# Performance work log

Measured on AMD Instinct MI355X. Metric: run time of the kernel, lower is better.

## Reference

```python
import jax, jax.numpy as jnp
import numpy as np

B, S, D, H = 2, 2048, 1024, 16
DH = D // H  # 64


def setup_inputs() -> dict:
    key = jax.random.key(0)
    ks = jax.random.split(key, 9)
    def rn(k, shape, scale=1.0):
        return jax.random.normal(k, shape, dtype=jnp.float32) * scale
    w_scale = 1.0 / np.sqrt(D)
    return {
        "queries": rn(ks[0], (B, S, D)),
        "keys": rn(ks[1], (B, S, D)),
        "values": rn(ks[2], (B, S, D)),
        "Wq": rn(ks[3], (D, D), w_scale),
        "bq": rn(ks[4], (D,), w_scale),
        "Wk": rn(ks[5], (D, D), w_scale),
        "bk": rn(ks[6], (D,), w_scale),
        "Wv": rn(ks[7], (D, D), w_scale),
        "bv": rn(ks[8], (D,), w_scale),
    }


def _split_heads(x):
    # torch: cat(split(x, DH, dim=-1), dim=0) -> index (h*B + b); equivalent to
    # [B,S,H,DH] -> [H,B,S,DH]
    bsz, slen, _ = x.shape
    return x.reshape(bsz, slen, H, DH).transpose(2, 0, 1, 3)


def reference(queries, keys, values, Wq, bq, Wk, bk, Wv, bv):
    # Linear projections (W stored so that y = x @ W + b)
    Q = queries @ Wq + bq
    K = keys @ Wk + bk
    V = values @ Wv + bv

    Qh = _split_heads(Q)  # [H,B,S,DH]
    Kh = _split_heads(K)
    Vh = _split_heads(V)

    scale = 1.0 / jnp.sqrt(jnp.asarray(DH, dtype=Qh.dtype))
    scores = jnp.einsum("hbqd,hbkd->hbqk", Qh, Kh) * scale  # [H,B,S,S]
    attn = jax.nn.softmax(scores, axis=-1)  # dropout_rate=0 -> identity
    out = jnp.einsum("hbqk,hbkd->hbqd", attn, Vh)  # [H,B,S,DH]

    # torch: cat(split(out, B, dim=0), dim=2) -> [B,S,H*DH] with head h in slice h
    out = out.transpose(1, 2, 0, 3).reshape(queries.shape[0], queries.shape[1], D)
    return out + queries  # residual; NOTE: W_O is defined but unused in the original forward
```

## Files before the change

### kernel.cpp

```cpp
#include <hip/hip_runtime.h>
#include <hip/hip_bf16.h>
#include <math.h>

#define BB 2
#define SS 2048
#define DD 1024
#define HH 16
#define DHH 64
#define MM (BB * SS)

typedef float f32x4 __attribute__((ext_vector_type(4)));
typedef float f32x16 __attribute__((ext_vector_type(16)));
typedef __bf16 bf16x8 __attribute__((ext_vector_type(8)));

#define N_QKV ((size_t)MM * DD)
#define N_W   ((size_t)DD * DD)

__device__ unsigned short g_X [3][N_QKV];
__device__ unsigned short g_Q [N_QKV];
__device__ unsigned short g_K [N_QKV];
__device__ unsigned short g_Vt[N_QKV];
__device__ unsigned short g_Wt[3][N_W];

__device__ __forceinline__ unsigned short f2bu(float f) {
    unsigned u = __float_as_uint(f);
    unsigned r = u + 0x7FFFu + ((u >> 16) & 1u);
    return (unsigned short)(r >> 16);
}

union FragU { uint4 u; bf16x8 v; unsigned short s[8]; };
static __device__ __forceinline__ bf16x8 ldfrag(const unsigned short* p) {
    FragU f; f.u = *(const uint4*)p; return f.v;
}

static __device__ __forceinline__ unsigned pkbf(float a, float b) {
    union { __bf16 h[2]; unsigned u; } w;
    w.h[0] = (__bf16)a; w.h[1] = (__bf16)b;
    return w.u;
}

__global__ __launch_bounds__(256) void cvt3(
        const float* __restrict__ x0, const float* __restrict__ x1,
        const float* __restrict__ x2, unsigned short* __restrict__ X)
{
    const float* src = blockIdx.y == 0 ? x0 : (blockIdx.y == 1 ? x1 : x2);
    unsigned short* dst = X + (size_t)blockIdx.y * N_QKV;
    const size_t i = ((size_t)blockIdx.x * 256 + threadIdx.x) * 4;
    const float4 v = *(const float4*)(src + i);
    ushort4 s;
    s.x = f2bu(v.x); s.y = f2bu(v.y); s.z = f2bu(v.z); s.w = f2bu(v.w);
    *(ushort4*)(dst + i) = s;
}

__global__ __launch_bounds__(256) void transpose_w3(
        const float* __restrict__ W0, const float* __restrict__ W1,
        const float* __restrict__ W2, unsigned short* __restrict__ Wt3)
{
    const float* W = blockIdx.z == 0 ? W0 : (blockIdx.z == 1 ? W1 : W2);
    unsigned short* Wt = Wt3 + (size_t)blockIdx.z * N_W;
    __shared__ float Ts[64][65];
    const int t = threadIdx.x;
    const int k0 = blockIdx.y * 64, n0 = blockIdx.x * 64;
#pragma unroll
    for (int i = 0; i < 16; ++i) {
        const int f = t + 256 * i, r = f >> 6, c = f & 63;
        Ts[r][c] = W[(size_t)(k0 + r) * DD + n0 + c];
    }
    __syncthreads();
#pragma unroll
    for (int i = 0; i < 16; ++i) {
        const int f = t + 256 * i, r = f >> 6, c = f & 63;
        Wt[(size_t)(n0 + r) * DD + k0 + c] = f2bu(Ts[c][r]);
    }
}

__global__ __launch_bounds__(256) void proj3(
        const unsigned short* __restrict__ X, const unsigned short* __restrict__ Wt3,
        const float* __restrict__ bq, const float* __restrict__ bk,
        const float* __restrict__ bv,
        unsigned short* __restrict__ Qp, unsigned short* __restrict__ Kp,
        unsigned short* __restrict__ Vtp)
{
    const int z = blockIdx.z;
    const unsigned short* xb = X   + (size_t)z * N_QKV;
    const unsigned short* Wt = Wt3 + (size_t)z * N_W;
    const float* bias = z == 0 ? bq : (z == 1 ? bk : bv);
    const float scale = z == 0 ? 0.18033688011112042f : 1.0f;

    __shared__ unsigned short As[128][72];
    __shared__ unsigned short Bs[128][72];
    const int t = threadIdx.x, lane = t & 63, w = t >> 6;
    const int q = lane >> 4, li = lane & 15;
    const int wm = (w >> 1) * 64, wn = (w & 1) * 64;
    const int m0 = blockIdx.y * 128, n0 = blockIdx.x * 128;
    const int rs = t >> 3, cs = (t & 7) * 8;

    f32x4 acc[4][4];
#pragma unroll
    for (int mt = 0; mt < 4; ++mt)
#pragma unroll
        for (int nt = 0; nt < 4; ++nt) acc[mt][nt] = (f32x4)0.f;

    uint4 pa0, pa1, pa2, pa3, pb0, pb1, pb2, pb3;
#define PROJ_LD(kk) \
    pa0 = *(const uint4*)(xb + (size_t)(m0 + rs      ) * DD + (kk) + cs); \
    pa1 = *(const uint4*)(xb + (size_t)(m0 + rs + 32 ) * DD + (kk) + cs); \
    pa2 = *(const uint4*)(xb + (size_t)(m0 + rs + 64 ) * DD + (kk) + cs); \
    pa3 = *(const uint4*)(xb + (size_t)(m0 + rs + 96 ) * DD + (kk) + cs); \
    pb0 = *(const uint4*)(Wt + (size_t)(n0 + rs      ) * DD + (kk) + cs); \
    pb1 = *(const uint4*)(Wt + (size_t)(n0 + rs + 32 ) * DD + (kk) + cs); \
    pb2 = *(const uint4*)(Wt + (size_t)(n0 + rs + 64 ) * DD + (kk) + cs); \
    pb3 = *(const uint4*)(Wt + (size_t)(n0 + rs + 96 ) * DD + (kk) + cs);

    PROJ_LD(0)

    for (int kk = 0; kk < DD; kk += 64) {
        *(uint4*)&As[rs     ][cs] = pa0;
        *(uint4*)&As[rs + 32][cs] = pa1;
        *(uint4*)&As[rs + 64][cs] = pa2;
        *(uint4*)&As[rs + 96][cs] = pa3;
        *(uint4*)&Bs[rs     ][cs] = pb0;
        *(uint4*)&Bs[rs + 32][cs] = pb1;
        *(uint4*)&Bs[rs + 64][cs] = pb2;
        *(uint4*)&Bs[rs + 96][cs] = pb3;
        __syncthreads();
        if (kk + 64 < DD) { PROJ_LD(kk + 64) }
#pragma unroll
        for (int ks = 0; ks < 64; ks += 32) {
            bf16x8 a[4], b[4];
#pragma unroll
            for (int mt = 0; mt < 4; ++mt) a[mt] = ldfrag(&As[wm + mt * 16 + li][ks + q * 8]);
#pragma unroll
            for (int nt = 0; nt < 4; ++nt) b[nt] = ldfrag(&Bs[wn + nt * 16 + li][ks + q * 8]);
#pragma unroll
            for (int mt = 0; mt < 4; ++mt)
#pragma unroll
                for (int nt = 0; nt < 4; ++nt)
                    acc[mt][nt] = __builtin_amdgcn_mfma_f32_16x16x32_bf16(
                        a[mt], b[nt], acc[mt][nt], 0, 0, 0);
        }
        __syncthreads();
    }
#undef PROJ_LD

    float bvv[4];
#pragma unroll
    for (int nt = 0; nt < 4; ++nt) bvv[nt] = bias[n0 + wn + nt * 16 + li];

    if (z < 2) {
        unsigned short* out = z == 0 ? Qp : Kp;
#pragma unroll
        for (int mt = 0; mt < 4; ++mt)
#pragma unroll
            for (int nt = 0; nt < 4; ++nt)
#pragma unroll
                for (int reg = 0; reg < 4; ++reg) {
                    const int m = m0 + wm + mt * 16 + q * 4 + reg;
                    out[(size_t)m * DD + n0 + wn + nt * 16 + li] =
                        f2bu((acc[mt][nt][reg] + bvv[nt]) * scale);
                }
    } else {
        const int b = m0 >> 11;
        const int h = (n0 + wn) >> 6;
#pragma unroll
        for (int mt = 0; mt < 4; ++mt)
#pragma unroll
            for (int nt = 0; nt < 4; ++nt) {
                const int s = (m0 & (SS - 1)) + wm + mt * 16 + q * 4;
                const int dh = nt * 16 + li;
                ushort4 sv;
                sv.x = f2bu(acc[mt][nt][0] + bvv[nt]);
                sv.y = f2bu(acc[mt][nt][1] + bvv[nt]);
                sv.z = f2bu(acc[mt][nt][2] + bvv[nt]);
                sv.w = f2bu(acc[mt][nt][3] + bvv[nt]);
                *(ushort4*)(Vtp + ((size_t)((b * HH + h) * DHH + dh)) * SS + s) = sv;
            }
    }
}

__global__ __launch_bounds__(256) void attn5(
        const unsigned short* __restrict__ Qg, const unsigned short* __restrict__ Kg,
        const unsigned short* __restrict__ Vtg,
        const float* __restrict__ queries, float* __restrict__ outp)
{
    __shared__ unsigned short Kb[2][64][64];
    __shared__ unsigned short Vb[2][64][64];
    __shared__ float invL[4][32];

    const int t = threadIdx.x, lane = t & 63, w = t >> 6;
    const int col = lane & 31;
    const int hi  = lane >> 5;
    const int qt = blockIdx.x, h = blockIdx.y, b = blockIdx.z;

    const int sr = t >> 3;
    const int sc = t & 7;

    const unsigned short* Kbase = Kg  + (size_t)(b * SS) * DD + h * DHH;
    const unsigned short* Vbase = Vtg + ((size_t)((b * HH + h) * DHH)) * SS;

    bf16x8 qa[4];
    {
        const unsigned short* qp =
            Qg + (size_t)(b * SS + qt * 128 + w * 32 + col) * DD + h * DHH + hi * 8;
#pragma unroll
        for (int i = 0; i < 4; ++i) qa[i] = ldfrag(qp + i * 16);
    }

    f32x16 o0 = (f32x16)0.f, o1 = (f32x16)0.f;
    float lsum = 0.f;

    uint4 k0, k1, v0, v1;
#define LD_TILE(s0) \
    k0 = *(const uint4*)(Kbase + (size_t)((s0) + sr     ) * DD + sc * 8); \
    k1 = *(const uint4*)(Kbase + (size_t)((s0) + sr + 32) * DD + sc * 8); \
    v0 = *(const uint4*)(Vbase + (size_t)(sr     ) * SS + (s0) + sc * 8); \
    v1 = *(const uint4*)(Vbase + (size_t)(sr + 32) * SS + (s0) + sc * 8);

#define ST_TILE(buf) \
    *(uint4*)&Kb[buf][sr     ][(sc ^ (sr & 7)) * 8] = k0; \
    *(uint4*)&Kb[buf][sr + 32][(sc ^ (sr & 7)) * 8] = k1; \
    *(uint4*)&Vb[buf][sr     ][(sc ^ (sr & 7)) * 8] = v0; \
    *(uint4*)&Vb[buf][sr + 32][(sc ^ (sr & 7)) * 8] = v1;

    LD_TILE(0)
    ST_TILE(0)
    __syncthreads();

    const int NT = SS / 64;
    for (int kt = 0; kt < NT; ++kt) {
        const int cur = kt & 1;
        if (kt + 1 < NT) { LD_TILE((kt + 1) * 64) }

#pragma unroll
        for (int ksub = 0; ksub < 2; ++ksub) {
            f32x16 st = (f32x16)0.f;
            const int krow = ksub * 32 + col;
#pragma unroll
            for (int i = 0; i < 4; ++i) {
                bf16x8 ka = ldfrag(&Kb[cur][krow][((i * 2 + hi) ^ (krow & 7)) * 8]);
                st = __builtin_amdgcn_mfma_f32_32x32x16_bf16(ka, qa[i], st, 0, 0, 0);
            }

            float pe[16];
#pragma unroll
            for (int r = 0; r < 16; ++r) { pe[r] = exp2f(st[r]); lsum += pe[r]; }

            unsigned wl[2][2], wh[2][2];
#pragma unroll
            for (int s = 0; s < 2; ++s) {
                wl[s][0] = pkbf(pe[8 * s + 0], pe[8 * s + 1]);
                wl[s][1] = pkbf(pe[8 * s + 2], pe[8 * s + 3]);
                wh[s][0] = pkbf(pe[8 * s + 4], pe[8 * s + 5]);
                wh[s][1] = pkbf(pe[8 * s + 6], pe[8 * s + 7]);
            }

            if (ksub == 0 && kt + 1 < NT) { ST_TILE(cur ^ 1) }

#pragma unroll
            for (int s = 0; s < 2; ++s) {
                const unsigned self0 = hi ? wh[s][0] : wl[s][0];
                const unsigned self1 = hi ? wh[s][1] : wl[s][1];
                const unsigned send0 = hi ? wl[s][0] : wh[s][0];
                const unsigned send1 = hi ? wl[s][1] : wh[s][1];
                const unsigned r0 = (unsigned)__shfl_xor((int)send0, 32);
                const unsigned r1 = (unsigned)__shfl_xor((int)send1, 32);
                FragU pf;
                pf.u.x = hi ? r0 : self0;
                pf.u.y = hi ? r1 : self1;
                pf.u.z = hi ? self0 : r0;
                pf.u.w = hi ? self1 : r1;

                const int vslot = ksub * 4 + s * 2 + hi;
                bf16x8 vb0 = ldfrag(&Vb[cur][col     ][(vslot ^ (col & 7)) * 8]);
                bf16x8 vb1 = ldfrag(&Vb[cur][col + 32][(vslot ^ (col & 7)) * 8]);
                o0 = __builtin_amdgcn_mfma_f32_32x32x16_bf16(pf.v, vb0, o0, 0, 0, 0);
                o1 = __builtin_amdgcn_mfma_f32_32x32x16_bf16(pf.v, vb1, o1, 0, 0, 0);
            }
        }
        __syncthreads();
    }
#undef LD_TILE
#undef ST_TILE

    const float lt = lsum + __shfl_xor(lsum, 32);
    if (lane < 32) invL[w][lane] = 1.f / lt;
    __syncthreads();

    const size_t gbase = (size_t)(b * SS + qt * 128 + w * 32) * DD + h * DHH + col;
#pragma unroll
    for (int reg = 0; reg < 16; ++reg) {
        const int rl = (reg & 3) + 8 * (reg >> 2) + 4 * hi;
        const float inv = invL[w][rl];
        const size_t g = gbase + (size_t)rl * DD;
        outp[g]      = o0[reg] * inv + queries[g];
        outp[g + 32] = o1[reg] * inv + queries[g + 32];
    }
}

extern "C" void kernel_launch(void* const* d_in, const int* in_sizes, int n_in,
                              void* d_out, int out_size, void* d_ws, size_t ws_size,
                              hipStream_t stream) {
    const float* queries = (const float*)d_in[0];
    const float* keys    = (const float*)d_in[1];
    const float* values  = (const float*)d_in[2];
    const float* Wq      = (const float*)d_in[3];
    const float* bq      = (const float*)d_in[4];
    const float* Wk      = (const float*)d_in[5];
    const float* bk      = (const float*)d_in[6];
    const float* Wv      = (const float*)d_in[7];
    const float* bv      = (const float*)d_in[8];
    float* outp = (float*)d_out;

    const size_t need = (6 * N_QKV + 3 * N_W) * sizeof(unsigned short);
    unsigned short *Xp, *Qp, *Kp, *Vtp, *Wtp;
    if (ws_size >= need) {
        Xp  = (unsigned short*)d_ws;
        Qp  = Xp + 3 * N_QKV;
        Kp  = Qp + N_QKV;
        Vtp = Kp + N_QKV;
        Wtp = Vtp + N_QKV;
    } else {
        hipGetSymbolAddress((void**)&Xp,  HIP_SYMBOL(g_X));
        hipGetSymbolAddress((void**)&Qp,  HIP_SYMBOL(g_Q));
        hipGetSymbolAddress((void**)&Kp,  HIP_SYMBOL(g_K));
        hipGetSymbolAddress((void**)&Vtp, HIP_SYMBOL(g_Vt));
        hipGetSymbolAddress((void**)&Wtp, HIP_SYMBOL(g_Wt));
    }

    const dim3 bp(256);
    cvt3<<<dim3(MM * DD / 1024, 3), bp, 0, stream>>>(queries, keys, values, Xp);
    transpose_w3<<<dim3(16, 16, 3), bp, 0, stream>>>(Wq, Wk, Wv, Wtp);
    proj3<<<dim3(8, 32, 3), bp, 0, stream>>>(Xp, Wtp, bq, bk, bv, Qp, Kp, Vtp);
    attn5<<<dim3(SS / 128, HH, BB), bp, 0, stream>>>(Qp, Kp, Vtp, queries, outp);
}
```

Baseline: 220.6 us.

## Restructure attention inner loop with paired QK MFMAs and permlane32 swaps

```diff
diff --git a/kernel.cpp b/kernel.cpp
--- a/kernel.cpp
+++ b/kernel.cpp
@@ -12,6 +12,7 @@
 typedef float f32x4 __attribute__((ext_vector_type(4)));
 typedef float f32x16 __attribute__((ext_vector_type(16)));
 typedef __bf16 bf16x8 __attribute__((ext_vector_type(8)));
+typedef unsigned int u32x2 __attribute__((ext_vector_type(2)));
 
 #define N_QKV ((size_t)MM * DD)
 #define N_W   ((size_t)DD * DD)
@@ -37,6 +38,28 @@
     union { __bf16 h[2]; unsigned u; } w;
     w.h[0] = (__bf16)a; w.h[1] = (__bf16)b;
     return w.u;
+}
+
+static __device__ __forceinline__ float fexp2(float x) {
+#if __has_builtin(__builtin_amdgcn_exp2f)
+    return __builtin_amdgcn_exp2f(x);
+#else
+    return __expf(x * 0.6931471805599453f);
+#endif
+}
+
+static __device__ __forceinline__ void plswap(unsigned &a, unsigned &b) {
+#if __has_builtin(__builtin_amdgcn_permlane32_swap)
+    u32x2 r = __builtin_amdgcn_permlane32_swap((int)a, (int)b, false, false);
+    a = r[0]; b = r[1];
+#else
+    const bool hi = (threadIdx.x & 63) >= 32;
+    unsigned x = hi ? a : b;
+    unsigned y = (unsigned)__shfl_xor((int)x, 32);
+    unsigned na = hi ? y : a;
+    unsigned nb = hi ? b : y;
+    a = na; b = nb;
+#endif
 }
 
 __global__ __launch_bounds__(256) void cvt3(
@@ -178,7 +201,7 @@
     }
 }
 
-__global__ __launch_bounds__(256) void attn5(
+__global__ __launch_bounds__(256) void attn6(
         const unsigned short* __restrict__ Qg, const unsigned short* __restrict__ Kg,
         const unsigned short* __restrict__ Vtg,
         const float* __restrict__ queries, float* __restrict__ outp)
@@ -208,6 +231,7 @@
 
     f32x16 o0 = (f32x16)0.f, o1 = (f32x16)0.f;
     float lsum = 0.f;
+    const int xr = col & 7;
 
     uint4 k0, k1, v0, v1;
 #define LD_TILE(s0) \
@@ -227,55 +251,61 @@
     __syncthreads();
 
     const int NT = SS / 64;
+#pragma unroll 2
     for (int kt = 0; kt < NT; ++kt) {
         const int cur = kt & 1;
         if (kt + 1 < NT) { LD_TILE((kt + 1) * 64) }
 
-#pragma unroll
-        for (int ksub = 0; ksub < 2; ++ksub) {
-            f32x16 st = (f32x16)0.f;
-            const int krow = ksub * 32 + col;
-#pragma unroll
-            for (int i = 0; i < 4; ++i) {
-                bf16x8 ka = ldfrag(&Kb[cur][krow][((i * 2 + hi) ^ (krow & 7)) * 8]);
-                st = __builtin_amdgcn_mfma_f32_32x32x16_bf16(ka, qa[i], st, 0, 0, 0);
+        f32x16 st0 = (f32x16)0.f, st1 = (f32x16)0.f;
+#pragma unroll
+        for (int i = 0; i < 4; ++i) {
+            const int slot = ((i * 2 + hi) ^ xr) * 8;
+            bf16x8 ka0 = ldfrag(&Kb[cur][col     ][slot]);
+            bf16x8 ka1 = ldfrag(&Kb[cur][col + 32][slot]);
+            st0 = __builtin_amdgcn_mfma_f32_32x32x16_bf16(ka0, qa[i], st0, 0, 0, 0);
+            st1 = __builtin_amdgcn_mfma_f32_32x32x16_bf16(ka1, qa[i], st1, 0, 0, 0);
+        }
+
+        unsigned pkw[4][4];
+        {
+            float pe0[16], pe1[16];
+#pragma unroll
+            for (int r = 0; r < 16; ++r) { pe0[r] = fexp2(st0[r]); }
+#pragma unroll
+            for (int r = 0; r < 16; ++r) { pe1[r] = fexp2(st1[r]); }
+            float ls = 0.f;
+#pragma unroll
+            for (int r = 0; r < 16; ++r) ls += pe0[r] + pe1[r];
+            lsum += ls;
+#pragma unroll
+            for (int s = 0; s < 2; ++s) {
+                pkw[s][0]     = pkbf(pe0[8 * s + 0], pe0[8 * s + 1]);
+                pkw[s][1]     = pkbf(pe0[8 * s + 2], pe0[8 * s + 3]);
+                pkw[s][2]     = pkbf(pe0[8 * s + 4], pe0[8 * s + 5]);
+                pkw[s][3]     = pkbf(pe0[8 * s + 6], pe0[8 * s + 7]);
+                pkw[2 + s][0] = pkbf(pe1[8 * s + 0], pe1[8 * s + 1]);
+                pkw[2 + s][1] = pkbf(pe1[8 * s + 2], pe1[8 * s + 3]);
+                pkw[2 + s][2] = pkbf(pe1[8 * s + 4], pe1[8 * s + 5]);
+                pkw[2 + s][3] = pkbf(pe1[8 * s + 6], pe1[8 * s + 7]);
             }
-
-            float pe[16];
-#pragma unroll
-            for (int r = 0; r < 16; ++r) { pe[r] = exp2f(st[r]); lsum += pe[r]; }
-
-            unsigned wl[2][2], wh[2][2];
-#pragma unroll
-            for (int s = 0; s < 2; ++s) {
-                wl[s][0] = pkbf(pe[8 * s + 0], pe[8 * s + 1]);
-                wl[s][1] = pkbf(pe[8 * s + 2], pe[8 * s + 3]);
-                wh[s][0] = pkbf(pe[8 * s + 4], pe[8 * s + 5]);
-                wh[s][1] = pkbf(pe[8 * s + 6], pe[8 * s + 7]);
-            }
-
-            if (ksub == 0 && kt + 1 < NT) { ST_TILE(cur ^ 1) }
-
-#pragma unroll
-            for (int s = 0; s < 2; ++s) {
-                const unsigned self0 = hi ? wh[s][0] : wl[s][0];
-                const unsigned self1 = hi ? wh[s][1] : wl[s][1];
-                const unsigned send0 = hi ? wl[s][0] : wh[s][0];
-                const unsigned send1 = hi ? wl[s][1] : wh[s][1];
-                const unsigned r0 = (unsigned)__shfl_xor((int)send0, 32);
-                const unsigned r1 = (unsigned)__shfl_xor((int)send1, 32);
-                FragU pf;
-                pf.u.x = hi ? r0 : self0;
-                pf.u.y = hi ? r1 : self1;
-                pf.u.z = hi ? self0 : r0;
-                pf.u.w = hi ? self1 : r1;
-
-                const int vslot = ksub * 4 + s * 2 + hi;
-                bf16x8 vb0 = ldfrag(&Vb[cur][col     ][(vslot ^ (col & 7)) * 8]);
-                bf16x8 vb1 = ldfrag(&Vb[cur][col + 32][(vslot ^ (col & 7)) * 8]);
-                o0 = __builtin_amdgcn_mfma_f32_32x32x16_bf16(pf.v, vb0, o0, 0, 0, 0);
-                o1 = __builtin_amdgcn_mfma_f32_32x32x16_bf16(pf.v, vb1, o1, 0, 0, 0);
-            }
+        }
+
+        if (kt + 1 < NT) { ST_TILE(cur ^ 1) }
+
+#pragma unroll
+        for (int c = 0; c < 4; ++c) {
+            unsigned a0 = pkw[c][0], b0 = pkw[c][2];
+            unsigned a1 = pkw[c][1], b1 = pkw[c][3];
+            plswap(a0, b0);
+            plswap(a1, b1);
+            FragU pf;
+            pf.u.x = a0; pf.u.y = a1; pf.u.z = b0; pf.u.w = b1;
+
+            const int vs = ((c * 2 + hi) ^ xr) * 8;
+            bf16x8 vb0 = ldfrag(&Vb[cur][col     ][vs]);
+            bf16x8 vb1 = ldfrag(&Vb[cur][col + 32][vs]);
+            o0 = __builtin_amdgcn_mfma_f32_32x32x16_bf16(pf.v, vb0, o0, 0, 0, 0);
+            o1 = __builtin_amdgcn_mfma_f32_32x32x16_bf16(pf.v, vb1, o1, 0, 0, 0);
         }
         __syncthreads();
     }
@@ -331,5 +361,5 @@
     cvt3<<<dim3(MM * DD / 1024, 3), bp, 0, stream>>>(queries, keys, values, Xp);
     transpose_w3<<<dim3(16, 16, 3), bp, 0, stream>>>(Wq, Wk, Wv, Wtp);
     proj3<<<dim3(8, 32, 3), bp, 0, stream>>>(Xp, Wtp, bq, bk, bv, Qp, Kp, Vtp);
-    attn5<<<dim3(SS / 128, HH, BB), bp, 0, stream>>>(Qp, Kp, Vtp, queries, outp);
-}
+    attn6<<<dim3(SS / 128, HH, BB), bp, 0, stream>>>(Qp, Kp, Vtp, queries, outp);
+}
```

Measured after the change: 205.9 us. 1.07x faster.
